# Optimization experiments

Measured on AMD Instinct MI355X. Metric: run time of the kernel, lower is better.

Reference implementation:

```python
import jax, jax.numpy as jnp
import numpy as np

N = 20000      # nodes
K = 32         # avg degree
E = N * K      # edges
H = 128        # num_hidden
NV = 128       # num_V
NE = 128       # num_E
NH = 4         # num_heads (hard-coded in module)
D = H // NH    # per-head dim


def setup_inputs() -> dict:
    key = jax.random.key(0)
    ks = jax.random.split(key, 16)
    w = lambda k, shape: jax.random.normal(k, shape, jnp.float32) * 0.02
    return {
        "h_V": jax.random.normal(ks[0], (N, NV), jnp.float32),
        "h_E": jax.random.normal(ks[1], (E, NE), jnp.float32),
        "edge_idx": jax.random.randint(ks[2], (2, E), 0, N, dtype=jnp.int64),
        # W_V: Linear(num_E, num_hidden) + GELU
        "Wv_w": w(ks[3], (H, NE)), "Wv_b": jnp.zeros((H,), jnp.float32),
        # Bias MLP: Linear(2*num_V+num_E, H) -> ReLU -> Linear(H, H) -> ReLU -> Linear(H, NH)
        "B1_w": w(ks[4], (H, 2 * NV + NE)), "B1_b": jnp.zeros((H,), jnp.float32),
        "B2_w": w(ks[5], (H, H)), "B2_b": jnp.zeros((H,), jnp.float32),
        "B3_w": w(ks[6], (NH, H)), "B3_b": jnp.zeros((NH,), jnp.float32),
        # W_O: Linear(H, num_V, bias=False); gate: Linear(H, num_V)
        "Wo_w": w(ks[7], (NV, H)),
        "gate_w": w(ks[8], (NV, H)), "gate_b": jnp.zeros((NV,), jnp.float32),
    }


def reference(h_V, h_E, edge_idx, Wv_w, Wv_b, B1_w, B1_b, B2_w, B2_b, B3_w, B3_b, Wo_w, gate_w, gate_b):
    src = edge_idx[0]
    dst = edge_idx[1]
    num_nodes = h_V.shape[0]

    # per-edge attention logits via small MLP on [h_V[src], h_E, h_V[dst]]
    cat = jnp.concatenate([h_V[src], h_E, h_V[dst]], axis=-1)          # [E, 2*NV+NE]
    x = jax.nn.relu(cat @ B1_w.T + B1_b)
    x = jax.nn.relu(x @ B2_w.T + B2_b)
    logits = (x @ B3_w.T + B3_b) / np.float32(np.sqrt(D))              # [E, NH]

    # per-edge values
    V = jax.nn.gelu(h_E @ Wv_w.T + Wv_b, approximate=False)           # [E, H]
    V = V.reshape(-1, NH, D)                                           # [E, NH, D]

    # scatter_softmax over edges grouped by src node
    m = jax.ops.segment_max(logits, src, num_segments=num_nodes)       # [N, NH]
    ex = jnp.exp(logits - m[src])                                      # [E, NH]
    denom = jax.ops.segment_sum(ex, src, num_segments=num_nodes)      # [N, NH]
    attend = ex / denom[src]                                           # [E, NH]

    # weighted scatter-sum aggregation
    agg = jax.ops.segment_sum(attend[:, :, None] * V, src, num_segments=num_nodes)
    agg = agg.reshape(num_nodes, -1)                                   # [N, H]

    h_V_gate = jax.nn.sigmoid(agg @ gate_w.T + gate_b)                 # [N, NV]
    dh = (agg @ Wo_w.T) * h_V_gate                                     # [N, NV]
    return h_V + dh
```

## Files before the change

kernel.cpp:

```cpp
#include <hip/hip_runtime.h>
#include <math.h>

typedef __attribute__((ext_vector_type(8))) short bf16x8;
typedef __attribute__((ext_vector_type(4))) float f32x4;
typedef unsigned short u16;

__device__ __forceinline__ short f2bf(float x) {
  union { float f; unsigned u; } c; c.f = x;
  unsigned u = c.u;
  u += 0x7fffu + ((u >> 16) & 1u);
  return (short)(u >> 16);
}
__device__ __forceinline__ float bf2f(u16 b) {
  union { unsigned u; float f; } c; c.u = ((unsigned)b) << 16; return c.f;
}
__device__ __forceinline__ unsigned pack2(float a, float b) {
  return ((unsigned)(u16)f2bf(a)) | (((unsigned)(u16)f2bf(b)) << 16);
}
__device__ __forceinline__ unsigned cvtpk(float lo, float hi) {
  unsigned r;
  asm("v_cvt_pk_bf16_f32 %0, %1, %2" : "=v"(r) : "v"(lo), "v"(hi));
  return r;
}
__device__ __forceinline__ float fast_erf(float x) {
// ... 54 lines not shown

__global__ void scatter_kernel(const int* __restrict__ src, const int* __restrict__ offs,
                               int* __restrict__ cur, int* __restrict__ order, int E) {
  int i = blockIdx.x * 256 + threadIdx.x;
  if (i >= E) return;
  int s = src[i];
  int p = offs[s] + atomicAdd(&cur[s], 1);
  order[p] = i;
}

__global__ void wcvt_kernel(const float* __restrict__ B1, const float* __restrict__ B2,
                            const float* __restrict__ B3, const float* __restrict__ Wv,
                            const float* __restrict__ Wo, const float* __restrict__ Wg,
                            short* __restrict__ o) {
  int i = blockIdx.x * 256 + threadIdx.x;
  if (i >= 115200) return;
  float val; int dst;
  if (i < 49152) {
    int row = i / 384, k = i % 384;
    val = B1[i];
    int c = k >> 5, s = (k >> 3) & 3, e = k & 7;
    dst = c * 4096 + row * 32 + ((s ^ ((row >> 1) & 3)) << 3) + e;
  } else if (i < 65536) {
    int j = i - 49152; int row = j >> 7, k = j & 127;
    val = B2[j];
    int c = k >> 5, s = (k >> 3) & 3, e = k & 7;
    dst = 49152 + c * 4096 + row * 32 + ((s ^ ((row >> 1) & 3)) << 3) + e;
  } else if (i < 66048) { val = B3[i - 65536]; dst = i; }
  else if (i < 82432) {
    int j = i - 66048; int row = j >> 7, k = j & 127;
    val = Wv[j];
    int c = k >> 5, s = (k >> 3) & 3, e = k & 7;
    dst = 66048 + c * 4096 + row * 32 + ((s ^ ((row >> 1) & 3)) << 3) + e;
  }
  else if (i < 98816)  { val = Wo[i - 82432]; dst = i; }
  else                 { val = Wg[i - 98816]; dst = i; }
  o[dst] = f2bf(val);
}

__global__ void cvtbf_kernel(const float* __restrict__ in, u16* __restrict__ out, long n8) {
  long i = (long)blockIdx.x * blockDim.x + threadIdx.x;
  long stride = (long)gridDim.x * blockDim.x;
  for (; i < n8; i += stride) {
    long b = i * 8;
    float4 a = *(const float4*)(in + b);
    float4 c = *(const float4*)(in + b + 4);
    uint4 u;
    u.x = pack2(a.x, a.y); u.y = pack2(a.z, a.w);
    u.z = pack2(c.x, c.y); u.w = pack2(c.z, c.w);
    *(uint4*)(out + b) = u;
  }
}

__global__ void __launch_bounds__(256, 3)
edge_kernel(const u16* __restrict__ hVb, const float* __restrict__ hE,
            const int* __restrict__ src, const int* __restrict__ dst,
            u16* __restrict__ Vout,
            const short* __restrict__ W1, const float* __restrict__ b1,
            const short* __restrict__ W2, const float* __restrict__ b2,
            const short* __restrict__ W3b, const float* __restrict__ b3,
            const short* __restrict__ Wv, const float* __restrict__ bv,
            float* __restrict__ logits, int E) {
  __shared__ u16 sE[64 * 128];
  __shared__ u16 sH[64 * 128];
  __shared__ u16 sW[2][4096];
  __shared__ float sPart[64][4][2];

  const int t = threadIdx.x;
  const int eBase = blockIdx.x * 64;
  const int lane = t & 63;
  const int wid = t >> 6;
  const int wrow = (wid >> 1) * 32;
  const int wcol = (wid & 1) * 64;
  const int lrow = lane & 15;
  const int kgrp = lane >> 4;

  auto STAGE = [&](const short* cp, int buf) {
#pragma unroll
    for (int i = 0; i < 2; ++i) {
      int L = t + i * 256;
      gload16(cp + L * 8, &sW[buf][L * 8]);
    }
  };

  STAGE(W1, 0);

#pragma unroll
  for (int i = 0; i < 4; ++i) {
    int u = t + i * 256;
    int row = u >> 4, sg = u & 15;
    const float* p = hE + (size_t)min(eBase + row, E - 1) * 128 + sg * 8;
    float4 f0 = *(const float4*)p;
    float4 f1 = *(const float4*)(p + 4);
    uint4 cv;
    cv.x = cvtpk(f0.x, f0.y); cv.y = cvtpk(f0.z, f0.w);
    cv.z = cvtpk(f1.x, f1.y); cv.w = cvtpk(f1.z, f1.w);
    *(uint4*)&sE[row * 128 + ((sg ^ (row & 15)) * 8)] = cv;
  }

  bf16x8 aS[4][2], aD[4][2];
  {
    int rS[2], rD[2];
#pragma unroll
    for (int mi = 0; mi < 2; ++mi) {
      int e = min(eBase + wrow + mi * 16 + lrow, E - 1);
      rS[mi] = src[e];
      rD[mi] = dst[e];
    }
#pragma unroll
    for (int c4 = 0; c4 < 4; ++c4) {
      const int kk = c4 * 32 + kgrp * 8;
#pragma unroll
      for (int mi = 0; mi < 2; ++mi) {
        aS[c4][mi] = *(const bf16x8*)(hVb + (size_t)rS[mi] * 128 + kk);
        aD[c4][mi] = *(const bf16x8*)(hVb + (size_t)rD[mi] * 128 + kk);
      }
    }
  }
  asm volatile("s_waitcnt vmcnt(0)" ::: "memory");
  __syncthreads();

  f32x4 acc[2][4];
  auto ZACC = [&]() {
#pragma unroll
    for (int mi = 0; mi < 2; ++mi)
#pragma unroll
      for (int nf = 0; nf < 4; ++nf)
#pragma unroll
        for (int q = 0; q < 4; ++q) acc[mi][nf][q] = 0.f;
  };
  auto LDSA = [&](const u16* s, int kk, bf16x8* a) {
#pragma unroll
    for (int mi = 0; mi < 2; ++mi) {
      int row = wrow + mi * 16 + lrow;
      int seg = (kk >> 3) ^ (row & 15);
      a[mi] = *(const bf16x8*)&s[row * 128 + seg * 8];
    }
  };
  auto STEP = [&](int buf, const short* nextCp, const bf16x8* a) {
    if (nextCp) STAGE(nextCp, buf ^ 1);
    bf16x8 b[4];
#pragma unroll
    for (int nf = 0; nf < 4; ++nf) {
      int row = wcol + nf * 16 + lrow;
      int seg = kgrp ^ ((row >> 1) & 3);
      b[nf] = *(const bf16x8*)&sW[buf][row * 32 + seg * 8];
    }
#pragma unroll
    for (int nf = 0; nf < 4; ++nf)
#pragma unroll
      for (int mi = 0; mi < 2; ++mi)
        acc[mi][nf] = __builtin_amdgcn_mfma_f32_16x16x32_bf16(a[mi], b[nf], acc[mi][nf], 0, 0, 0);
    if (nextCp) asm volatile("s_waitcnt vmcnt(0)" ::: "memory");
    __syncthreads();
  };

  ZACC();
  STEP(0, W1 + 1 * 4096, aS[0]);
  STEP(1, W1 + 2 * 4096, aS[1]);
  STEP(0, W1 + 3 * 4096, aS[2]);
  STEP(1, W1 + 4 * 4096, aS[3]);
#pragma unroll
  for (int c4 = 0; c4 < 4; ++c4) {
    bf16x8 a[2];
    LDSA(sE, c4 * 32 + kgrp * 8, a);
    STEP((4 + c4) & 1, W1 + (5 + c4) * 4096, a);
  }
  STEP(0, W1 + 9 * 4096, aD[0]);
  STEP(1, W1 + 10 * 4096, aD[1]);
  STEP(0, W1 + 11 * 4096, aD[2]);
  STEP(1, Wv, aD[3]);
  {
    float b1c[4];
#pragma unroll
    for (int nf = 0; nf < 4; ++nf) b1c[nf] = b1[wcol + nf * 16 + lrow];
#pragma unroll
    for (int mi = 0; mi < 2; ++mi)
#pragma unroll
      for (int nf = 0; nf < 4; ++nf)
#pragma unroll
        for (int q = 0; q < 4; ++q) {
          int row = wrow + mi * 16 + kgrp * 4 + q;
          int col = wcol + nf * 16 + lrow;
          int seg = (col >> 3) ^ (row & 15);
          sH[row * 128 + seg * 8 + (col & 7)] =
              (u16)f2bf(fmaxf(acc[mi][nf][q] + b1c[nf], 0.f));
        }
  }

  ZACC();
#pragma unroll
  for (int v = 0; v < 4; ++v) {
    bf16x8 a[2];
    LDSA(sE, v * 32 + kgrp * 8, a);
    const short* nxt = (v < 3) ? (Wv + (v + 1) * 4096) : W2;
    STEP(v & 1, nxt, a);
  }
  {
    float bvc[4];
#pragma unroll
    for (int nf = 0; nf < 4; ++nf) bvc[nf] = bv[wcol + nf * 16 + lrow];
#pragma unroll
    for (int mi = 0; mi < 2; ++mi)
#pragma unroll
      for (int nf = 0; nf < 4; ++nf)
#pragma unroll
        for (int q = 0; q < 4; ++q) {
          int row = wrow + mi * 16 + kgrp * 4 + q;
          int col = wcol + nf * 16 + lrow;
          float x = acc[mi][nf][q] + bvc[nf];
          float g = 0.5f * x * (1.0f + fast_erf(x * 0.70710678118654752f));
          int seg = (col >> 3) ^ (row & 15);
          sE[row * 128 + seg * 8 + (col & 7)] = (u16)f2bf(g);
        }
  }
  __syncthreads();
#pragma unroll
  for (int i = 0; i < 4; ++i) {
    int u = t + i * 256;
    int row = u >> 4, g16 = u & 15;
    int seg = g16 ^ (row & 15);
    uint4 v = *(const uint4*)&sE[row * 128 + seg * 8];
    int e = eBase + row;
    if (e < E) *(uint4*)(Vout + (size_t)e * 128 + g16 * 8) = v;
  }

  ZACC();
#pragma unroll
  for (int u = 0; u < 4; ++u) {
    bf16x8 a[2];
    LDSA(sH, u * 32 + kgrp * 8, a);
    const short* nxt = (u < 3) ? (W2 + (u + 1) * 4096) : nullptr;
    STEP(u & 1, nxt, a);
  }
  {
    float b2c[4], w3v[4][4];
#pragma unroll
    for (int nf = 0; nf < 4; ++nf) {
      int col = wcol + nf * 16 + lrow;
      b2c[nf] = b2[col];
#pragma unroll
      for (int h = 0; h < 4; ++h) w3v[h][nf] = bf2f((u16)W3b[h * 128 + col]);
    }
#pragma unroll
    for (int mi = 0; mi < 2; ++mi)
#pragma unroll
      for (int q = 0; q < 4; ++q) {
        float p0 = 0.f, p1 = 0.f, p2 = 0.f, p3 = 0.f;
#pragma unroll
        for (int nf = 0; nf < 4; ++nf) {
          float x = fmaxf(acc[mi][nf][q] + b2c[nf], 0.f);
          p0 += x * w3v[0][nf]; p1 += x * w3v[1][nf];
          p2 += x * w3v[2][nf]; p3 += x * w3v[3][nf];
        }
#pragma unroll
        for (int o = 1; o < 16; o <<= 1) {
          p0 += __shfl_xor(p0, o); p1 += __shfl_xor(p1, o);
          p2 += __shfl_xor(p2, o); p3 += __shfl_xor(p3, o);
        }
        if (lrow < 4) {
          float pw = (lrow == 0) ? p0 : (lrow == 1) ? p1 : (lrow == 2) ? p2 : p3;
          sPart[wrow + mi * 16 + kgrp * 4 + q][lrow][wid & 1] = pw;
        }
      }
  }
  __syncthreads();
  if (t < 64) {
    int e = eBase + t;
    if (e < E) {
      float4 lg;
      lg.x = (sPart[t][0][0] + sPart[t][0][1] + b3[0]) * 0.17677669529663687f;
      lg.y = (sPart[t][1][0] + sPart[t][1][1] + b3[1]) * 0.17677669529663687f;
      lg.z = (sPart[t][2][0] + sPart[t][2][1] + b3[2]) * 0.17677669529663687f;
      lg.w = (sPart[t][3][0] + sPart[t][3][1] + b3[3]) * 0.17677669529663687f;
      *(float4*)(logits + (size_t)e * 4) = lg;
    }
  }
}

__global__ void __launch_bounds__(256)
nm_kernel(const float* __restrict__ logits, const int* __restrict__ offs,
          const int* __restrict__ order, float* __restrict__ attw,
          float* __restrict__ inv, int nN) {
  const int wid = threadIdx.x >> 6, lane = threadIdx.x & 63;
  const int nW = gridDim.x * 4;
  for (int v = blockIdx.x * 4 + wid; v < nN; v += nW) {
    const int base = offs[v];
    const int deg = offs[v + 1] - base;
    float m0 = -3e38f, m1 = -3e38f, m2 = -3e38f, m3 = -3e38f;
    for (int i = lane; i < deg; i += 64) {
      int e = order[base + i];
      float4 l = *(const float4*)(logits + (size_t)e * 4);
      m0 = fmaxf(m0, l.x); m1 = fmaxf(m1, l.y);
      m2 = fmaxf(m2, l.z); m3 = fmaxf(m3, l.w);
    }
#pragma unroll
    for (int o = 32; o > 0; o >>= 1) {
      m0 = fmaxf(m0, __shfl_xor(m0, o)); m1 = fmaxf(m1, __shfl_xor(m1, o));
      m2 = fmaxf(m2, __shfl_xor(m2, o)); m3 = fmaxf(m3, __shfl_xor(m3, o));
    }
    float d0 = 0.f, d1 = 0.f, d2 = 0.f, d3 = 0.f;
    for (int i = lane; i < deg; i += 64) {
      int e = order[base + i];
      float4 l = *(const float4*)(logits + (size_t)e * 4);
      float4 ex;
      ex.x = __expf(l.x - m0); ex.y = __expf(l.y - m1);
      ex.z = __expf(l.z - m2); ex.w = __expf(l.w - m3);
      *(float4*)(attw + (size_t)e * 4) = ex;
      d0 += ex.x; d1 += ex.y; d2 += ex.z; d3 += ex.w;
    }
#pragma unroll
    for (int o = 32; o > 0; o >>= 1) {
      d0 += __shfl_xor(d0, o); d1 += __shfl_xor(d1, o);
      d2 += __shfl_xor(d2, o); d3 += __shfl_xor(d3, o);
    }
    if (lane < 4) {
      float dv = (lane == 0) ? d0 : (lane == 1) ? d1 : (lane == 2) ? d2 : d3;
      inv[(size_t)v * 4 + lane] = (dv > 0.f) ? 1.f / dv : 0.f;
    }
  }
}

__device__ __forceinline__ float dot8(const float* ag, uint4 w) {
  unsigned wr[4] = {w.x, w.y, w.z, w.w};
  float s = 0.f;
#pragma unroll
  for (int q = 0; q < 4; ++q) {
    s += ag[2 * q]     * bf2f((u16)(wr[q] & 0xffffu));
    s += ag[2 * q + 1] * bf2f((u16)(wr[q] >> 16));
// ... 90 lines not shown
  const float* B3w  = (const float*)d_in[9];
  const float* B3b  = (const float*)d_in[10];
  const float* WoW  = (const float*)d_in[11];
  const float* GW   = (const float*)d_in[12];
  const float* GB   = (const float*)d_in[13];

  const int Nn = in_sizes[0] / 128;
  const int E  = in_sizes[1] / 128;
  if (Nn <= 0 || E <= 0) return;

  char* ws = (char*)d_ws;
  size_t off = 0;
  auto alloc = [&](size_t b) { size_t o = off; off += (b + 255) & ~(size_t)255; return o; };
  const size_t o_idx   = alloc((size_t)2 * E * 4);
  const size_t o_cnt   = alloc((size_t)(Nn + 1) * 4);
  const size_t o_offs  = alloc((size_t)(Nn + 1) * 4);
  const size_t o_cur   = alloc((size_t)Nn * 4);
  const size_t o_order = alloc((size_t)E * 4);
  const size_t o_flag  = alloc(256);
  const size_t o_log   = alloc((size_t)E * 16);
  const size_t o_attw  = alloc((size_t)E * 16);
  const size_t o_inv   = alloc((size_t)Nn * 16);
  const size_t o_V     = alloc((size_t)E * 256);
  const size_t o_hVb   = alloc((size_t)Nn * 256);
  const size_t o_wbf   = alloc((size_t)115200 * 2);

  if (off > ws_size) {
    fb_kernel<<<(out_size + 255) / 256, 256, 0, stream>>>(hV, (float*)d_out, out_size);
    return;
  }

  int*   idx32  = (int*)(ws + o_idx);
  int*   cnt    = (int*)(ws + o_cnt);
  int*   offsP  = (int*)(ws + o_offs);
  int*   cur    = (int*)(ws + o_cur);
  int*   order  = (int*)(ws + o_order);
  int*   flag   = (int*)(ws + o_flag);
  float* logits = (float*)(ws + o_log);
  float* attw   = (float*)(ws + o_attw);
  float* invd   = (float*)(ws + o_inv);
  u16*   Vb     = (u16*)(ws + o_V);
  u16*   hVb    = (u16*)(ws + o_hVb);
  short* wbf    = (short*)(ws + o_wbf);

  short* W1b = wbf;
  short* W2b = wbf + 49152;
  short* W3b = wbf + 65536;
  short* Wvb = wbf + 66048;
  short* Wob = wbf + 82432;
  short* Wgb = wbf + 98816;

  const int* src = idx32;
  const int* dst = idx32 + E;

  detect_kernel<<<1, 256, 0, stream>>>((const unsigned*)eidx, flag);
  hipMemsetAsync(cnt, 0, (size_t)(Nn + 1) * 4, stream);
  hipMemsetAsync(cur, 0, (size_t)Nn * 4, stream);
  convert_count_kernel<<<(2 * E + 255) / 256, 256, 0, stream>>>(eidx, idx32, flag, cnt, E);
  scan_kernel<<<1, 1024, 0, stream>>>(cnt, offsP, Nn);
  scatter_kernel<<<(E + 255) / 256, 256, 0, stream>>>(src, offsP, cur, order, E);
  wcvt_kernel<<<(115200 + 255) / 256, 256, 0, stream>>>(B1w, B2w, B3w, WvW, WoW, GW, wbf);
  cvtbf_kernel<<<512, 256, 0, stream>>>(hV, hVb, (long)Nn * 16);

  edge_kernel<<<(E + 63) / 64, 256, 0, stream>>>(
      hVb, hE, src, dst, Vb, W1b, B1b, W2b, B2b, W3b, B3b, Wvb, WvB, logits, E);

  nm_kernel<<<(Nn + 3) / 4, 256, 0, stream>>>(logits, offsP, order, attw, invd, Nn);

  agg_kernel<<<1024, 256, 0, stream>>>(
      hV, attw, invd, Vb, offsP, order, Wob, Wgb, GB, (float*)d_out, Nn);
}
```

Measured before the change: 558.3 us.

## Deepen weight staging to four LDS buffers and interleave V and logits GEMMs

Switches the weight staging in the edge kernel from a double buffer with a full vmcnt(0) wait and barrier after every step to a four-deep ring buffer. Each step now waits on a partial vmcnt count, so several weight chunks stay in flight. The Wv GEMM is moved first and its GELU epilogue and V store are placed between W1 steps, which lets the sE and sH tiles share one LDS buffer. It also keeps two accumulator sets live at once, which raises register pressure and could hurt occupancy under the launch-bounds limit of 3.

Result: slower. 581.7 us (+4.2%).

```diff
diff --git a/kernel.cpp b/kernel.cpp
--- a/kernel.cpp
+++ b/kernel.cpp
@@ -130,6 +130,25 @@
   }
 }
 
+#define STEPK(N, BUF, NEXTP, NBUF, APTR, ACC)                                  \
+  do {                                                                         \
+    asm volatile("s_waitcnt vmcnt(" #N ")" ::: "memory");                      \
+    __builtin_amdgcn_sched_barrier(0);                                         \
+    __builtin_amdgcn_s_barrier();                                              \
+    __builtin_amdgcn_sched_barrier(0);                                         \
+    if (NEXTP) STAGE(NEXTP, NBUF);                                             \
+    bf16x8 b_[4];                                                              \
+    _Pragma("unroll") for (int nf_ = 0; nf_ < 4; ++nf_) {                      \
+      int row_ = wcol + nf_ * 16 + lrow;                                       \
+      int seg_ = kgrp ^ ((row_ >> 1) & 3);                                     \
+      b_[nf_] = *(const bf16x8*)&sW[BUF][row_ * 32 + seg_ * 8];                \
+    }                                                                          \
+    _Pragma("unroll") for (int nf_ = 0; nf_ < 4; ++nf_)                        \
+      _Pragma("unroll") for (int mi_ = 0; mi_ < 2; ++mi_)                      \
+        ACC[mi_][nf_] = __builtin_amdgcn_mfma_f32_16x16x32_bf16(               \
+            (APTR)[mi_], b_[nf_], ACC[mi_][nf_], 0, 0, 0);                     \
+  } while (0)
+
 __global__ void __launch_bounds__(256, 3)
 edge_kernel(const u16* __restrict__ hVb, const float* __restrict__ hE,
             const int* __restrict__ src, const int* __restrict__ dst,
@@ -139,9 +158,8 @@
             const short* __restrict__ W3b, const float* __restrict__ b3,
             const short* __restrict__ Wv, const float* __restrict__ bv,
             float* __restrict__ logits, int E) {
-  __shared__ u16 sE[64 * 128];
-  __shared__ u16 sH[64 * 128];
-  __shared__ u16 sW[2][4096];
+  __shared__ u16 sEH[64 * 128];
+  __shared__ u16 sW[4][4096];
   __shared__ float sPart[64][4][2];
 
   const int t = threadIdx.x;
@@ -161,7 +179,9 @@
     }
   };
 
-  STAGE(W1, 0);
+  STAGE(Wv, 0);
+  STAGE(Wv + 4096, 1);
+  STAGE(Wv + 2 * 4096, 2);
 
 #pragma unroll
   for (int i = 0; i < 4; ++i) {
@@ -173,7 +193,7 @@
     uint4 cv;
     cv.x = cvtpk(f0.x, f0.y); cv.y = cvtpk(f0.z, f0.w);
     cv.z = cvtpk(f1.x, f1.y); cv.w = cvtpk(f1.z, f1.w);
-    *(uint4*)&sE[row * 128 + ((sg ^ (row & 15)) * 8)] = cv;
+    *(uint4*)&sEH[row * 128 + ((sg ^ (row & 15)) * 8)] = cv;
   }
 
   bf16x8 aS[4][2], aD[4][2];
@@ -195,59 +215,78 @@
       }
     }
   }
-  asm volatile("s_waitcnt vmcnt(0)" ::: "memory");
-  __syncthreads();
-
-  f32x4 acc[2][4];
-  auto ZACC = [&]() {
+#pragma unroll
+  for (int c4 = 0; c4 < 4; ++c4)
 #pragma unroll
     for (int mi = 0; mi < 2; ++mi)
-#pragma unroll
-      for (int nf = 0; nf < 4; ++nf)
-#pragma unroll
-        for (int q = 0; q < 4; ++q) acc[mi][nf][q] = 0.f;
-  };
-  auto LDSA = [&](const u16* s, int kk, bf16x8* a) {
+      asm volatile("" :: "v"(aS[c4][mi]), "v"(aD[c4][mi]));
+  __syncthreads();
+
+  f32x4 accL[2][4], accV[2][4];
+#pragma unroll
+  for (int mi = 0; mi < 2; ++mi)
+#pragma unroll
+    for (int nf = 0; nf < 4; ++nf)
+#pragma unroll
+      for (int q = 0; q < 4; ++q) { accL[mi][nf][q] = 0.f; accV[mi][nf][q] = 0.f; }
+
+  auto LDSA = [&](int kk, bf16x8* a) {
 #pragma unroll
     for (int mi = 0; mi < 2; ++mi) {
       int row = wrow + mi * 16 + lrow;
       int seg = (kk >> 3) ^ (row & 15);
-      a[mi] = *(const bf16x8*)&s[row * 128 + seg * 8];
+      a[mi] = *(const bf16x8*)&sEH[row * 128 + seg * 8];
     }
   };
-  auto STEP = [&](int buf, const short* nextCp, const bf16x8* a) {
-    if (nextCp) STAGE(nextCp, buf ^ 1);
-    bf16x8 b[4];
-#pragma unroll
-    for (int nf = 0; nf < 4; ++nf) {
-      int row = wcol + nf * 16 + lrow;
-      int seg = kgrp ^ ((row >> 1) & 3);
-      b[nf] = *(const bf16x8*)&sW[buf][row * 32 + seg * 8];
-    }
-#pragma unroll
-    for (int nf = 0; nf < 4; ++nf)
-#pragma unroll
-      for (int mi = 0; mi < 2; ++mi)
-        acc[mi][nf] = __builtin_amdgcn_mfma_f32_16x16x32_bf16(a[mi], b[nf], acc[mi][nf], 0, 0, 0);
-    if (nextCp) asm volatile("s_waitcnt vmcnt(0)" ::: "memory");
-    __syncthreads();
-  };
-
-  ZACC();
-  STEP(0, W1 + 1 * 4096, aS[0]);
-  STEP(1, W1 + 2 * 4096, aS[1]);
-  STEP(0, W1 + 3 * 4096, aS[2]);
-  STEP(1, W1 + 4 * 4096, aS[3]);
-#pragma unroll
-  for (int c4 = 0; c4 < 4; ++c4) {
-    bf16x8 a[2];
-    LDSA(sE, c4 * 32 + kgrp * 8, a);
-    STEP((4 + c4) & 1, W1 + (5 + c4) * 4096, a);
-  }
-  STEP(0, W1 + 9 * 4096, aD[0]);
-  STEP(1, W1 + 10 * 4096, aD[1]);
-  STEP(0, W1 + 11 * 4096, aD[2]);
-  STEP(1, Wv, aD[3]);
+
+  { bf16x8 a_[2]; LDSA(0 * 32 + kgrp * 8, a_); STEPK(4, 0, Wv + 3 * 4096, 3, a_, accV); }
+  { bf16x8 a_[2]; LDSA(1 * 32 + kgrp * 8, a_); STEPK(4, 1, W1 + 4 * 4096, 0, a_, accV); }
+  { bf16x8 a_[2]; LDSA(2 * 32 + kgrp * 8, a_); STEPK(4, 2, W1 + 5 * 4096, 1, a_, accV); }
+  { bf16x8 a_[2]; LDSA(3 * 32 + kgrp * 8, a_); STEPK(4, 3, W1 + 6 * 4096, 2, a_, accV); }
+  { bf16x8 a_[2]; LDSA(0 * 32 + kgrp * 8, a_); STEPK(4, 0, W1 + 7 * 4096, 3, a_, accL); }
+  { bf16x8 a_[2]; LDSA(1 * 32 + kgrp * 8, a_); STEPK(4, 1, W1 + 0 * 4096, 0, a_, accL); }
+  { bf16x8 a_[2]; LDSA(2 * 32 + kgrp * 8, a_); STEPK(4, 2, W1 + 1 * 4096, 1, a_, accL); }
+  { bf16x8 a_[2]; LDSA(3 * 32 + kgrp * 8, a_); STEPK(4, 3, W1 + 2 * 4096, 2, a_, accL); }
+  STEPK(4, 0, W1 + 3 * 4096, 3, aS[0], accL);
+
+  {
+    float bvc[4];
+#pragma unroll
+    for (int nf = 0; nf < 4; ++nf) bvc[nf] = bv[wcol + nf * 16 + lrow];
+#pragma unroll
+    for (int mi = 0; mi < 2; ++mi)
+#pragma unroll
+      for (int nf = 0; nf < 4; ++nf)
+#pragma unroll
+        for (int q = 0; q < 4; ++q) {
+          int row = wrow + mi * 16 + kgrp * 4 + q;
+          int col = wcol + nf * 16 + lrow;
+          float x = accV[mi][nf][q] + bvc[nf];
+          float g = 0.5f * x * (1.0f + fast_erf(x * 0.70710678118654752f));
+          int seg = (col >> 3) ^ (row & 15);
+          sEH[row * 128 + seg * 8 + (col & 7)] = (u16)f2bf(g);
+        }
+  }
+
+  STEPK(4, 1, W1 + 8 * 4096, 0, aS[1], accL);
+  STEPK(4, 2, W1 + 9 * 4096, 1, aS[2], accL);
+
+#pragma unroll
+  for (int i = 0; i < 4; ++i) {
+    int u = t + i * 256;
+    int row = u >> 4, g16 = u & 15;
+    int seg = g16 ^ (row & 15);
+    uint4 v = *(const uint4*)&sEH[row * 128 + seg * 8];
+    int e = eBase + row;
+    if (e < E) *(uint4*)(Vout + (size_t)e * 128 + g16 * 8) = v;
+  }
+
+  STEPK(8, 3, W1 + 10 * 4096, 2, aS[3], accL);
+  STEPK(8, 0, W1 + 11 * 4096, 3, aD[0], accL);
+  STEPK(8, 1, W2 + 0 * 4096, 0, aD[1], accL);
+  STEPK(4, 2, W2 + 1 * 4096, 1, aD[2], accL);
+  STEPK(4, 3, W2 + 2 * 4096, 2, aD[3], accL);
+
   {
     float b1c[4];
 #pragma unroll
@@ -261,56 +300,23 @@
           int row = wrow + mi * 16 + kgrp * 4 + q;
           int col = wcol + nf * 16 + lrow;
           int seg = (col >> 3) ^ (row & 15);
-          sH[row * 128 + seg * 8 + (col & 7)] =
-              (u16)f2bf(fmaxf(acc[mi][nf][q] + b1c[nf], 0.f));
+          sEH[row * 128 + seg * 8 + (col & 7)] =
+              (u16)f2bf(fmaxf(accL[mi][nf][q] + b1c[nf], 0.f));
         }
-  }
-
-  ZACC();
-#pragma unroll
-  for (int v = 0; v < 4; ++v) {
-    bf16x8 a[2];
-    LDSA(sE, v * 32 + kgrp * 8, a);
-    const short* nxt = (v < 3) ? (Wv + (v + 1) * 4096) : W2;
-    STEP(v & 1, nxt, a);
-  }
-  {
-    float bvc[4];
-#pragma unroll
-    for (int nf = 0; nf < 4; ++nf) bvc[nf] = bv[wcol + nf * 16 + lrow];
 #pragma unroll
     for (int mi = 0; mi < 2; ++mi)
 #pragma unroll
       for (int nf = 0; nf < 4; ++nf)
 #pragma unroll
-        for (int q = 0; q < 4; ++q) {
-          int row = wrow + mi * 16 + kgrp * 4 + q;
-          int col = wcol + nf * 16 + lrow;
-          float x = acc[mi][nf][q] + bvc[nf];
-          float g = 0.5f * x * (1.0f + fast_erf(x * 0.70710678118654752f));
-          int seg = (col >> 3) ^ (row & 15);
-          sE[row * 128 + seg * 8 + (col & 7)] = (u16)f2bf(g);
-        }
-  }
-  __syncthreads();
-#pragma unroll
-  for (int i = 0; i < 4; ++i) {
-    int u = t + i * 256;
-    int row = u >> 4, g16 = u & 15;
-    int seg = g16 ^ (row & 15);
-    uint4 v = *(const uint4*)&sE[row * 128 + seg * 8];
-    int e = eBase + row;
-    if (e < E) *(uint4*)(Vout + (size_t)e * 128 + g16 * 8) = v;
-  }
-
-  ZACC();
-#pragma unroll
-  for (int u = 0; u < 4; ++u) {
-    bf16x8 a[2];
-    LDSA(sH, u * 32 + kgrp * 8, a);
-    const short* nxt = (u < 3) ? (W2 + (u + 1) * 4096) : nullptr;
-    STEP(u & 1, nxt, a);
-  }
+        for (int q = 0; q < 4; ++q) accV[mi][nf][q] = 0.f;
+  }
+  __syncthreads();
+
+  { bf16x8 a_[2]; LDSA(0 * 32 + kgrp * 8, a_); STEPK(4, 0, W2 + 3 * 4096, 3, a_, accV); }
+  { bf16x8 a_[2]; LDSA(1 * 32 + kgrp * 8, a_); STEPK(4, 1, (const short*)nullptr, 0, a_, accV); }
+  { bf16x8 a_[2]; LDSA(2 * 32 + kgrp * 8, a_); STEPK(2, 2, (const short*)nullptr, 0, a_, accV); }
+  { bf16x8 a_[2]; LDSA(3 * 32 + kgrp * 8, a_); STEPK(0, 3, (const short*)nullptr, 0, a_, accV); }
+
   {
     float b2c[4], w3v[4][4];
 #pragma unroll
@@ -327,7 +333,7 @@
         float p0 = 0.f, p1 = 0.f, p2 = 0.f, p3 = 0.f;
 #pragma unroll
         for (int nf = 0; nf < 4; ++nf) {
-          float x = fmaxf(acc[mi][nf][q] + b2c[nf], 0.f);
+          float x = fmaxf(accV[mi][nf][q] + b2c[nf], 0.f);
           p0 += x * w3v[0][nf]; p1 += x * w3v[1][nf];
           p2 += x * w3v[2][nf]; p3 += x * w3v[3][nf];
         }
```

## Triple-buffer weight staging with counted vmcnt waits in edge kernel

Applied to the files above, without the earlier changes.

Replaces the double-buffered weight staging with a three-slot ring, where each step waits with a partial vmcnt, issues one barrier, then prefetches the tile two steps ahead. The goal is to keep more global loads in flight and cut per-step full drains and the trailing barrier. Bias and W3 values are now loaded once up front and pinned in registers, so they no longer load between GEMM phases. The cost is more LDS per block and higher register pressure, which may hurt the three-blocks-per-CU occupancy target, and the hand-counted vmcnt values are fragile.

Result: slower. 641.8 us (+15.0%).

```diff
diff --git a/kernel.cpp b/kernel.cpp
--- a/kernel.cpp
+++ b/kernel.cpp
@@ -130,6 +130,25 @@
   }
 }
 
+#define PSTEP(N, BUF, NEXTP, NBUF, APTR)                                       \
+  do {                                                                         \
+    asm volatile("s_waitcnt vmcnt(" #N ")" ::: "memory");                      \
+    __builtin_amdgcn_sched_barrier(0);                                         \
+    __builtin_amdgcn_s_barrier();                                              \
+    __builtin_amdgcn_sched_barrier(0);                                         \
+    if (NEXTP) STAGE((const short*)(NEXTP), NBUF);                             \
+    bf16x8 b_[4];                                                              \
+    _Pragma("unroll") for (int nf_ = 0; nf_ < 4; ++nf_) {                      \
+      int row_ = wcol + nf_ * 16 + lrow;                                       \
+      int seg_ = kgrp ^ ((row_ >> 1) & 3);                                     \
+      b_[nf_] = *(const bf16x8*)&sW[BUF][row_ * 32 + seg_ * 8];                \
+    }                                                                          \
+    _Pragma("unroll") for (int nf_ = 0; nf_ < 4; ++nf_)                        \
+      _Pragma("unroll") for (int mi_ = 0; mi_ < 2; ++mi_)                      \
+        acc[mi_][nf_] = __builtin_amdgcn_mfma_f32_16x16x32_bf16(               \
+            (APTR)[mi_], b_[nf_], acc[mi_][nf_], 0, 0, 0);                     \
+  } while (0)
+
 __global__ void __launch_bounds__(256, 3)
 edge_kernel(const u16* __restrict__ hVb, const float* __restrict__ hE,
             const int* __restrict__ src, const int* __restrict__ dst,
@@ -141,7 +160,7 @@
             float* __restrict__ logits, int E) {
   __shared__ u16 sE[64 * 128];
   __shared__ u16 sH[64 * 128];
-  __shared__ u16 sW[2][4096];
+  __shared__ u16 sW[3][4096];
   __shared__ float sPart[64][4][2];
 
   const int t = threadIdx.x;
@@ -162,6 +181,7 @@
   };
 
   STAGE(W1, 0);
+  STAGE(W1 + 4096, 1);
 
 #pragma unroll
   for (int i = 0; i < 4; ++i) {
@@ -195,7 +215,27 @@
       }
     }
   }
+  float b1c[4], bvc[4], b2c[4], w3v[4][4];
+#pragma unroll
+  for (int nf = 0; nf < 4; ++nf) {
+    int col = wcol + nf * 16 + lrow;
+    b1c[nf] = b1[col]; bvc[nf] = bv[col]; b2c[nf] = b2[col];
+#pragma unroll
+    for (int h = 0; h < 4; ++h) w3v[h][nf] = bf2f((u16)W3b[h * 128 + col]);
+  }
+#pragma unroll
+  for (int c4 = 0; c4 < 4; ++c4)
+#pragma unroll
+    for (int mi = 0; mi < 2; ++mi)
+      asm volatile("" :: "v"(aS[c4][mi]), "v"(aD[c4][mi]));
+#pragma unroll
+  for (int nf = 0; nf < 4; ++nf) {
+    asm volatile("" :: "v"(b1c[nf]), "v"(bvc[nf]), "v"(b2c[nf]));
+#pragma unroll
+    for (int h = 0; h < 4; ++h) asm volatile("" :: "v"(w3v[h][nf]));
+  }
   asm volatile("s_waitcnt vmcnt(0)" ::: "memory");
+  __builtin_amdgcn_sched_barrier(0);
   __syncthreads();
 
   f32x4 acc[2][4];
@@ -215,83 +255,54 @@
       a[mi] = *(const bf16x8*)&s[row * 128 + seg * 8];
     }
   };
-  auto STEP = [&](int buf, const short* nextCp, const bf16x8* a) {
-    if (nextCp) STAGE(nextCp, buf ^ 1);
-    bf16x8 b[4];
-#pragma unroll
-    for (int nf = 0; nf < 4; ++nf) {
-      int row = wcol + nf * 16 + lrow;
-      int seg = kgrp ^ ((row >> 1) & 3);
-      b[nf] = *(const bf16x8*)&sW[buf][row * 32 + seg * 8];
-    }
+
+  ZACC();
+  PSTEP(2, 0, W1 + 2 * 4096, 2, aS[0]);
+  PSTEP(2, 1, W1 + 3 * 4096, 0, aS[1]);
+  PSTEP(2, 2, W1 + 4 * 4096, 1, aS[2]);
+  PSTEP(2, 0, W1 + 5 * 4096, 2, aS[3]);
+  { bf16x8 a_[2]; LDSA(sE, 0 * 32 + kgrp * 8, a_); PSTEP(2, 1, W1 + 6 * 4096, 0, a_); }
+  { bf16x8 a_[2]; LDSA(sE, 1 * 32 + kgrp * 8, a_); PSTEP(2, 2, W1 + 7 * 4096, 1, a_); }
+  { bf16x8 a_[2]; LDSA(sE, 2 * 32 + kgrp * 8, a_); PSTEP(2, 0, W1 + 8 * 4096, 2, a_); }
+  { bf16x8 a_[2]; LDSA(sE, 3 * 32 + kgrp * 8, a_); PSTEP(2, 1, W1 + 9 * 4096, 0, a_); }
+  PSTEP(2, 2, W1 + 10 * 4096, 1, aD[0]);
+  PSTEP(2, 0, W1 + 11 * 4096, 2, aD[1]);
+  PSTEP(2, 1, Wv, 0, aD[2]);
+  PSTEP(2, 2, Wv + 4096, 1, aD[3]);
+
+#pragma unroll
+  for (int mi = 0; mi < 2; ++mi)
 #pragma unroll
     for (int nf = 0; nf < 4; ++nf)
 #pragma unroll
-      for (int mi = 0; mi < 2; ++mi)
-        acc[mi][nf] = __builtin_amdgcn_mfma_f32_16x16x32_bf16(a[mi], b[nf], acc[mi][nf], 0, 0, 0);
-    if (nextCp) asm volatile("s_waitcnt vmcnt(0)" ::: "memory");
-    __syncthreads();
-  };
+      for (int q = 0; q < 4; ++q) {
+        int row = wrow + mi * 16 + kgrp * 4 + q;
+        int col = wcol + nf * 16 + lrow;
+        int seg = (col >> 3) ^ (row & 15);
+        sH[row * 128 + seg * 8 + (col & 7)] =
+            (u16)f2bf(fmaxf(acc[mi][nf][q] + b1c[nf], 0.f));
+      }
 
   ZACC();
-  STEP(0, W1 + 1 * 4096, aS[0]);
-  STEP(1, W1 + 2 * 4096, aS[1]);
-  STEP(0, W1 + 3 * 4096, aS[2]);
-  STEP(1, W1 + 4 * 4096, aS[3]);
-#pragma unroll
-  for (int c4 = 0; c4 < 4; ++c4) {
-    bf16x8 a[2];
-    LDSA(sE, c4 * 32 + kgrp * 8, a);
-    STEP((4 + c4) & 1, W1 + (5 + c4) * 4096, a);
-  }
-  STEP(0, W1 + 9 * 4096, aD[0]);
-  STEP(1, W1 + 10 * 4096, aD[1]);
-  STEP(0, W1 + 11 * 4096, aD[2]);
-  STEP(1, Wv, aD[3]);
-  {
-    float b1c[4];
-#pragma unroll
-    for (int nf = 0; nf < 4; ++nf) b1c[nf] = b1[wcol + nf * 16 + lrow];
-#pragma unroll
-    for (int mi = 0; mi < 2; ++mi)
-#pragma unroll
-      for (int nf = 0; nf < 4; ++nf)
-#pragma unroll
-        for (int q = 0; q < 4; ++q) {
-          int row = wrow + mi * 16 + kgrp * 4 + q;
-          int col = wcol + nf * 16 + lrow;
-          int seg = (col >> 3) ^ (row & 15);
-          sH[row * 128 + seg * 8 + (col & 7)] =
-              (u16)f2bf(fmaxf(acc[mi][nf][q] + b1c[nf], 0.f));
-        }
-  }
-
-  ZACC();
-#pragma unroll
-  for (int v = 0; v < 4; ++v) {
-    bf16x8 a[2];
-    LDSA(sE, v * 32 + kgrp * 8, a);
-    const short* nxt = (v < 3) ? (Wv + (v + 1) * 4096) : W2;
-    STEP(v & 1, nxt, a);
-  }
-  {
-    float bvc[4];
-#pragma unroll
-    for (int nf = 0; nf < 4; ++nf) bvc[nf] = bv[wcol + nf * 16 + lrow];
-#pragma unroll
-    for (int mi = 0; mi < 2; ++mi)
-#pragma unroll
-      for (int nf = 0; nf < 4; ++nf)
-#pragma unroll
-        for (int q = 0; q < 4; ++q) {
-          int row = wrow + mi * 16 + kgrp * 4 + q;
-          int col = wcol + nf * 16 + lrow;
-          float x = acc[mi][nf][q] + bvc[nf];
-          float g = 0.5f * x * (1.0f + fast_erf(x * 0.70710678118654752f));
-          int seg = (col >> 3) ^ (row & 15);
-          sE[row * 128 + seg * 8 + (col & 7)] = (u16)f2bf(g);
-        }
-  }
+  { bf16x8 a_[2]; LDSA(sE, 0 * 32 + kgrp * 8, a_); PSTEP(2, 0, Wv + 2 * 4096, 2, a_); }
+  { bf16x8 a_[2]; LDSA(sE, 1 * 32 + kgrp * 8, a_); PSTEP(2, 1, Wv + 3 * 4096, 0, a_); }
+  { bf16x8 a_[2]; LDSA(sE, 2 * 32 + kgrp * 8, a_); PSTEP(2, 2, W2, 1, a_); }
+  { bf16x8 a_[2]; LDSA(sE, 3 * 32 + kgrp * 8, a_); PSTEP(2, 0, W2 + 4096, 2, a_); }
+  __syncthreads();
+
+#pragma unroll
+  for (int mi = 0; mi < 2; ++mi)
+#pragma unroll
+    for (int nf = 0; nf < 4; ++nf)
+#pragma unroll
+      for (int q = 0; q < 4; ++q) {
+        int row = wrow + mi * 16 + kgrp * 4 + q;
+        int col = wcol + nf * 16 + lrow;
+        float x = acc[mi][nf][q] + bvc[nf];
+        float g = 0.5f * x * (1.0f + fast_erf(x * 0.70710678118654752f));
+        int seg = (col >> 3) ^ (row & 15);
+        sE[row * 128 + seg * 8 + (col & 7)] = (u16)f2bf(g);
+      }
   __syncthreads();
 #pragma unroll
   for (int i = 0; i < 4; ++i) {
@@ -304,22 +315,12 @@
   }
 
   ZACC();
-#pragma unroll
-  for (int u = 0; u < 4; ++u) {
-    bf16x8 a[2];
-    LDSA(sH, u * 32 + kgrp * 8, a);
-    const short* nxt = (u < 3) ? (W2 + (u + 1) * 4096) : nullptr;
-    STEP(u & 1, nxt, a);
-  }
+  { bf16x8 a_[2]; LDSA(sH, 0 * 32 + kgrp * 8, a_); PSTEP(6, 1, W2 + 2 * 4096, 0, a_); }
+  { bf16x8 a_[2]; LDSA(sH, 1 * 32 + kgrp * 8, a_); PSTEP(6, 2, W2 + 3 * 4096, 1, a_); }
+  { bf16x8 a_[2]; LDSA(sH, 2 * 32 + kgrp * 8, a_); PSTEP(2, 0, (const short*)0, 0, a_); }
+  { bf16x8 a_[2]; LDSA(sH, 3 * 32 + kgrp * 8, a_); PSTEP(0, 1, (const short*)0, 0, a_); }
+
   {
-    float b2c[4], w3v[4][4];
-#pragma unroll
-    for (int nf = 0; nf < 4; ++nf) {
-      int col = wcol + nf * 16 + lrow;
-      b2c[nf] = b2[col];
-#pragma unroll
-      for (int h = 0; h < 4; ++h) w3v[h][nf] = bf2f((u16)W3b[h * 128 + col]);
-    }
 #pragma unroll
     for (int mi = 0; mi < 2; ++mi)
 #pragma unroll
```

## Split edge kernel into persistent logits and V-projection kernels with LDS-resident weights

Applied to the files above, without the earlier changes.

Replaces the single per-tile edge kernel, which re-streamed every weight chunk from global memory per 64-edge tile, with two persistent grid-stride kernels. The logits kernel keeps all of W1 and W2 resident in LDS (about 130KB) across tiles. The V projection kernel keeps Wv resident and runs at higher occupancy. This removes the repeated weight staging and per-chunk barriers. In exchange hE is read from global twice, and the logits kernel runs one 512-thread block per CU with no overlap of gather loads and compute.

Result: slower. 705.8 us (+26.4%).

```diff
diff --git a/kernel.cpp b/kernel.cpp
--- a/kernel.cpp
+++ b/kernel.cpp
@@ -130,158 +130,260 @@
   }
 }
 
-__global__ void __launch_bounds__(256, 3)
-edge_kernel(const u16* __restrict__ hVb, const float* __restrict__ hE,
-            const int* __restrict__ src, const int* __restrict__ dst,
-            u16* __restrict__ Vout,
-            const short* __restrict__ W1, const float* __restrict__ b1,
-            const short* __restrict__ W2, const float* __restrict__ b2,
-            const short* __restrict__ W3b, const float* __restrict__ b3,
-            const short* __restrict__ Wv, const float* __restrict__ bv,
-            float* __restrict__ logits, int E) {
-  __shared__ u16 sE[64 * 128];
-  __shared__ u16 sH[64 * 128];
-  __shared__ u16 sW[2][4096];
-  __shared__ float sPart[64][4][2];
+__global__ void __launch_bounds__(512, 1)
+logits_kernel(const u16* __restrict__ hVb, const float* __restrict__ hE,
+              const int* __restrict__ src, const int* __restrict__ dst,
+              const short* __restrict__ W1, const float* __restrict__ b1,
+              const short* __restrict__ W2, const float* __restrict__ b2,
+              const short* __restrict__ W3b, const float* __restrict__ b3,
+              float* __restrict__ logits, int E, int nTiles) {
+  __shared__ u16 sW1[49152];
+  __shared__ u16 sW2[16384];
+  __shared__ u16 sEH[8192];
+  __shared__ float sPart[64][4][4];
 
   const int t = threadIdx.x;
-  const int eBase = blockIdx.x * 64;
   const int lane = t & 63;
   const int wid = t >> 6;
-  const int wrow = (wid >> 1) * 32;
-  const int wcol = (wid & 1) * 64;
+  const int wrow = (wid >> 2) * 32;
+  const int wcol = (wid & 3) * 32;
   const int lrow = lane & 15;
   const int kgrp = lane >> 4;
 
-  auto STAGE = [&](const short* cp, int buf) {
-#pragma unroll
-    for (int i = 0; i < 2; ++i) {
-      int L = t + i * 256;
-      gload16(cp + L * 8, &sW[buf][L * 8]);
-    }
-  };
-
-  STAGE(W1, 0);
-
+#pragma unroll
+  for (int i = 0; i < 12; ++i) {
+    int L = t + i * 512;
+    gload16(W1 + L * 8, &sW1[L * 8]);
+  }
 #pragma unroll
   for (int i = 0; i < 4; ++i) {
-    int u = t + i * 256;
-    int row = u >> 4, sg = u & 15;
-    const float* p = hE + (size_t)min(eBase + row, E - 1) * 128 + sg * 8;
-    float4 f0 = *(const float4*)p;
-    float4 f1 = *(const float4*)(p + 4);
-    uint4 cv;
-    cv.x = cvtpk(f0.x, f0.y); cv.y = cvtpk(f0.z, f0.w);
-    cv.z = cvtpk(f1.x, f1.y); cv.w = cvtpk(f1.z, f1.w);
-    *(uint4*)&sE[row * 128 + ((sg ^ (row & 15)) * 8)] = cv;
-  }
-
-  bf16x8 aS[4][2], aD[4][2];
-  {
-    int rS[2], rD[2];
-#pragma unroll
-    for (int mi = 0; mi < 2; ++mi) {
-      int e = min(eBase + wrow + mi * 16 + lrow, E - 1);
-      rS[mi] = src[e];
-      rD[mi] = dst[e];
-    }
-#pragma unroll
-    for (int c4 = 0; c4 < 4; ++c4) {
-      const int kk = c4 * 32 + kgrp * 8;
-#pragma unroll
-      for (int mi = 0; mi < 2; ++mi) {
-        aS[c4][mi] = *(const bf16x8*)(hVb + (size_t)rS[mi] * 128 + kk);
-        aD[c4][mi] = *(const bf16x8*)(hVb + (size_t)rD[mi] * 128 + kk);
-      }
-    }
-  }
+    int L = t + i * 512;
+    gload16(W2 + L * 8, &sW2[L * 8]);
+  }
+  float b1c[2], b2c[2], w3v[4][2];
+#pragma unroll
+  for (int nf = 0; nf < 2; ++nf) {
+    int col = wcol + nf * 16 + lrow;
+    b1c[nf] = b1[col]; b2c[nf] = b2[col];
+#pragma unroll
+    for (int h = 0; h < 4; ++h) w3v[h][nf] = bf2f((u16)W3b[h * 128 + col]);
+  }
+  const float b3c0 = b3[0], b3c1 = b3[1], b3c2 = b3[2], b3c3 = b3[3];
   asm volatile("s_waitcnt vmcnt(0)" ::: "memory");
   __syncthreads();
 
-  f32x4 acc[2][4];
+  f32x4 acc[2][2];
   auto ZACC = [&]() {
 #pragma unroll
     for (int mi = 0; mi < 2; ++mi)
 #pragma unroll
-      for (int nf = 0; nf < 4; ++nf)
+      for (int nf = 0; nf < 2; ++nf)
 #pragma unroll
         for (int q = 0; q < 4; ++q) acc[mi][nf][q] = 0.f;
   };
-  auto LDSA = [&](const u16* s, int kk, bf16x8* a) {
+  auto LDSA = [&](int kk, bf16x8* a) {
 #pragma unroll
     for (int mi = 0; mi < 2; ++mi) {
       int row = wrow + mi * 16 + lrow;
       int seg = (kk >> 3) ^ (row & 15);
-      a[mi] = *(const bf16x8*)&s[row * 128 + seg * 8];
+      a[mi] = *(const bf16x8*)&sEH[row * 128 + seg * 8];
     }
   };
-  auto STEP = [&](int buf, const short* nextCp, const bf16x8* a) {
-    if (nextCp) STAGE(nextCp, buf ^ 1);
-    bf16x8 b[4];
-#pragma unroll
-    for (int nf = 0; nf < 4; ++nf) {
-      int row = wcol + nf * 16 + lrow;
-      int seg = kgrp ^ ((row >> 1) & 3);
-      b[nf] = *(const bf16x8*)&sW[buf][row * 32 + seg * 8];
-    }
-#pragma unroll
-    for (int nf = 0; nf < 4; ++nf)
-#pragma unroll
-      for (int mi = 0; mi < 2; ++mi)
-        acc[mi][nf] = __builtin_amdgcn_mfma_f32_16x16x32_bf16(a[mi], b[nf], acc[mi][nf], 0, 0, 0);
-    if (nextCp) asm volatile("s_waitcnt vmcnt(0)" ::: "memory");
-    __syncthreads();
-  };
-
-  ZACC();
-  STEP(0, W1 + 1 * 4096, aS[0]);
-  STEP(1, W1 + 2 * 4096, aS[1]);
-  STEP(0, W1 + 3 * 4096, aS[2]);
-  STEP(1, W1 + 4 * 4096, aS[3]);
-#pragma unroll
-  for (int c4 = 0; c4 < 4; ++c4) {
-    bf16x8 a[2];
-    LDSA(sE, c4 * 32 + kgrp * 8, a);
-    STEP((4 + c4) & 1, W1 + (5 + c4) * 4096, a);
-  }
-  STEP(0, W1 + 9 * 4096, aD[0]);
-  STEP(1, W1 + 10 * 4096, aD[1]);
-  STEP(0, W1 + 11 * 4096, aD[2]);
-  STEP(1, Wv, aD[3]);
-  {
-    float b1c[4];
-#pragma unroll
-    for (int nf = 0; nf < 4; ++nf) b1c[nf] = b1[wcol + nf * 16 + lrow];
+
+  for (int tile = blockIdx.x; tile < nTiles; tile += gridDim.x) {
+    const int eBase = tile * 64;
+#pragma unroll
+    for (int i = 0; i < 2; ++i) {
+      int u = t + i * 512;
+      int row = u >> 4, sg = u & 15;
+      const float* p = hE + (size_t)min(eBase + row, E - 1) * 128 + sg * 8;
+      float4 f0 = *(const float4*)p;
+      float4 f1 = *(const float4*)(p + 4);
+      uint4 cv;
+      cv.x = cvtpk(f0.x, f0.y); cv.y = cvtpk(f0.z, f0.w);
+      cv.z = cvtpk(f1.x, f1.y); cv.w = cvtpk(f1.z, f1.w);
+      *(uint4*)&sEH[row * 128 + ((sg ^ (row & 15)) * 8)] = cv;
+    }
+    bf16x8 aS[4][2], aD[4][2];
+    {
+      int rS[2], rD[2];
+#pragma unroll
+      for (int mi = 0; mi < 2; ++mi) {
+        int e = min(eBase + wrow + mi * 16 + lrow, E - 1);
+        rS[mi] = src[e]; rD[mi] = dst[e];
+      }
+#pragma unroll
+      for (int c4 = 0; c4 < 4; ++c4) {
+        int kk = c4 * 32 + kgrp * 8;
+#pragma unroll
+        for (int mi = 0; mi < 2; ++mi) {
+          aS[c4][mi] = *(const bf16x8*)(hVb + (size_t)rS[mi] * 128 + kk);
+          aD[c4][mi] = *(const bf16x8*)(hVb + (size_t)rD[mi] * 128 + kk);
+        }
+      }
+    }
+    __syncthreads();
+
+    ZACC();
+#pragma unroll
+    for (int c = 0; c < 12; ++c) {
+      bf16x8 a[2], b[2];
+      if (c < 4)      { a[0] = aS[c][0]; a[1] = aS[c][1]; }
+      else if (c < 8) { LDSA((c - 4) * 32 + kgrp * 8, a); }
+      else            { a[0] = aD[c - 8][0]; a[1] = aD[c - 8][1]; }
+#pragma unroll
+      for (int nf = 0; nf < 2; ++nf) {
+        int row_ = wcol + nf * 16 + lrow;
+        b[nf] = *(const bf16x8*)&sW1[c * 4096 + row_ * 32 + ((kgrp ^ ((row_ >> 1) & 3)) << 3)];
+      }
+#pragma unroll
+      for (int nf = 0; nf < 2; ++nf)
+#pragma unroll
+        for (int mi = 0; mi < 2; ++mi)
+          acc[mi][nf] = __builtin_amdgcn_mfma_f32_16x16x32_bf16(a[mi], b[nf], acc[mi][nf], 0, 0, 0);
+    }
+    __syncthreads();
+
 #pragma unroll
     for (int mi = 0; mi < 2; ++mi)
 #pragma unroll
-      for (int nf = 0; nf < 4; ++nf)
+      for (int nf = 0; nf < 2; ++nf)
 #pragma unroll
         for (int q = 0; q < 4; ++q) {
           int row = wrow + mi * 16 + kgrp * 4 + q;
           int col = wcol + nf * 16 + lrow;
           int seg = (col >> 3) ^ (row & 15);
-          sH[row * 128 + seg * 8 + (col & 7)] =
+          sEH[row * 128 + seg * 8 + (col & 7)] =
               (u16)f2bf(fmaxf(acc[mi][nf][q] + b1c[nf], 0.f));
         }
-  }
-
-  ZACC();
-#pragma unroll
-  for (int v = 0; v < 4; ++v) {
-    bf16x8 a[2];
-    LDSA(sE, v * 32 + kgrp * 8, a);
-    const short* nxt = (v < 3) ? (Wv + (v + 1) * 4096) : W2;
-    STEP(v & 1, nxt, a);
-  }
-  {
-    float bvc[4];
-#pragma unroll
-    for (int nf = 0; nf < 4; ++nf) bvc[nf] = bv[wcol + nf * 16 + lrow];
+    __syncthreads();
+
+    ZACC();
+#pragma unroll
+    for (int c = 0; c < 4; ++c) {
+      bf16x8 a[2], b[2];
+      LDSA(c * 32 + kgrp * 8, a);
+#pragma unroll
+      for (int nf = 0; nf < 2; ++nf) {
+        int row_ = wcol + nf * 16 + lrow;
+        b[nf] = *(const bf16x8*)&sW2[c * 4096 + row_ * 32 + ((kgrp ^ ((row_ >> 1) & 3)) << 3)];
+      }
+#pragma unroll
+      for (int nf = 0; nf < 2; ++nf)
+#pragma unroll
+        for (int mi = 0; mi < 2; ++mi)
+          acc[mi][nf] = __builtin_amdgcn_mfma_f32_16x16x32_bf16(a[mi], b[nf], acc[mi][nf], 0, 0, 0);
+    }
+
 #pragma unroll
     for (int mi = 0; mi < 2; ++mi)
 #pragma unroll
-      for (int nf = 0; nf < 4; ++nf)
+      for (int q = 0; q < 4; ++q) {
+        float p0 = 0.f, p1 = 0.f, p2 = 0.f, p3 = 0.f;
+#pragma unroll
+        for (int nf = 0; nf < 2; ++nf) {
+          float x = fmaxf(acc[mi][nf][q] + b2c[nf], 0.f);
+          p0 += x * w3v[0][nf]; p1 += x * w3v[1][nf];
+          p2 += x * w3v[2][nf]; p3 += x * w3v[3][nf];
+        }
+#pragma unroll
+        for (int o = 1; o < 16; o <<= 1) {
+          p0 += __shfl_xor(p0, o); p1 += __shfl_xor(p1, o);
+          p2 += __shfl_xor(p2, o); p3 += __shfl_xor(p3, o);
+        }
+        if (lrow < 4) {
+          float pw = (lrow == 0) ? p0 : (lrow == 1) ? p1 : (lrow == 2) ? p2 : p3;
+          sPart[wrow + mi * 16 + kgrp * 4 + q][lrow][wid & 3] = pw;
+        }
+      }
+    __syncthreads();
+    if (t < 256) {
+      int r = t >> 2, h = t & 3;
+      float bb = (h == 0) ? b3c0 : (h == 1) ? b3c1 : (h == 2) ? b3c2 : b3c3;
+      float lg = (sPart[r][h][0] + sPart[r][h][1] + sPart[r][h][2] + sPart[r][h][3] + bb)
+                 * 0.17677669529663687f;
+      int e = eBase + r;
+      if (e < E) logits[(size_t)e * 4 + h] = lg;
+    }
+    __syncthreads();
+  }
+}
+
+__global__ void __launch_bounds__(512, 3)
+vproj_kernel(const float* __restrict__ hE, const short* __restrict__ Wv,
+             const float* __restrict__ bv, u16* __restrict__ Vout,
+             int E, int nTiles) {
+  __shared__ u16 sWv[16384];
+  __shared__ u16 sE[8192];
+
+  const int t = threadIdx.x;
+  const int lane = t & 63;
+  const int wid = t >> 6;
+  const int wrow = (wid >> 2) * 32;
+  const int wcol = (wid & 3) * 32;
+  const int lrow = lane & 15;
+  const int kgrp = lane >> 4;
+
+#pragma unroll
+  for (int i = 0; i < 4; ++i) {
+    int L = t + i * 512;
+    gload16(Wv + L * 8, &sWv[L * 8]);
+  }
+  float bvc[2];
+#pragma unroll
+  for (int nf = 0; nf < 2; ++nf) bvc[nf] = bv[wcol + nf * 16 + lrow];
+  asm volatile("s_waitcnt vmcnt(0)" ::: "memory");
+  __syncthreads();
+
+  f32x4 acc[2][2];
+  for (int tile = blockIdx.x; tile < nTiles; tile += gridDim.x) {
+    const int eBase = tile * 64;
+#pragma unroll
+    for (int i = 0; i < 2; ++i) {
+      int u = t + i * 512;
+      int row = u >> 4, sg = u & 15;
+      const float* p = hE + (size_t)min(eBase + row, E - 1) * 128 + sg * 8;
+      float4 f0 = *(const float4*)p;
+      float4 f1 = *(const float4*)(p + 4);
+      uint4 cv;
+      cv.x = cvtpk(f0.x, f0.y); cv.y = cvtpk(f0.z, f0.w);
+      cv.z = cvtpk(f1.x, f1.y); cv.w = cvtpk(f1.z, f1.w);
+      *(uint4*)&sE[row * 128 + ((sg ^ (row & 15)) * 8)] = cv;
+    }
+    __syncthreads();
+
+#pragma unroll
+    for (int mi = 0; mi < 2; ++mi)
+#pragma unroll
+      for (int nf = 0; nf < 2; ++nf)
+#pragma unroll
+        for (int q = 0; q < 4; ++q) acc[mi][nf][q] = 0.f;
+#pragma unroll
+    for (int c = 0; c < 4; ++c) {
+      bf16x8 a[2], b[2];
+#pragma unroll
+      for (int mi = 0; mi < 2; ++mi) {
+        int row = wrow + mi * 16 + lrow;
+        int seg = ((c * 32 + kgrp * 8) >> 3) ^ (row & 15);
+        a[mi] = *(const bf16x8*)&sE[row * 128 + seg * 8];
+      }
+#pragma unroll
+      for (int nf = 0; nf < 2; ++nf) {
+        int row_ = wcol + nf * 16 + lrow;
+        b[nf] = *(const bf16x8*)&sWv[c * 4096 + row_ * 32 + ((kgrp ^ ((row_ >> 1) & 3)) << 3)];
+      }
+#pragma unroll
+      for (int nf = 0; nf < 2; ++nf)
+#pragma unroll
+        for (int mi = 0; mi < 2; ++mi)
+          acc[mi][nf] = __builtin_amdgcn_mfma_f32_16x16x32_bf16(a[mi], b[nf], acc[mi][nf], 0, 0, 0);
+    }
+    __syncthreads();
+
+#pragma unroll
+    for (int mi = 0; mi < 2; ++mi)
+#pragma unroll
+      for (int nf = 0; nf < 2; ++nf)
 #pragma unroll
         for (int q = 0; q < 4; ++q) {
           int row = wrow + mi * 16 + kgrp * 4 + q;
@@ -291,68 +393,17 @@
           int seg = (col >> 3) ^ (row & 15);
           sE[row * 128 + seg * 8 + (col & 7)] = (u16)f2bf(g);
         }
-  }
-  __syncthreads();
-#pragma unroll
-  for (int i = 0; i < 4; ++i) {
-    int u = t + i * 256;
-    int row = u >> 4, g16 = u & 15;
-    int seg = g16 ^ (row & 15);
-    uint4 v = *(const uint4*)&sE[row * 128 + seg * 8];
-    int e = eBase + row;
-    if (e < E) *(uint4*)(Vout + (size_t)e * 128 + g16 * 8) = v;
-  }
-
-  ZACC();
-#pragma unroll
-  for (int u = 0; u < 4; ++u) {
-    bf16x8 a[2];
-    LDSA(sH, u * 32 + kgrp * 8, a);
-    const short* nxt = (u < 3) ? (W2 + (u + 1) * 4096) : nullptr;
-    STEP(u & 1, nxt, a);
-  }
-  {
-    float b2c[4], w3v[4][4];
-#pragma unroll
-    for (int nf = 0; nf < 4; ++nf) {
-      int col = wcol + nf * 16 + lrow;
-      b2c[nf] = b2[col];
-#pragma unroll
-      for (int h = 0; h < 4; ++h) w3v[h][nf] = bf2f((u16)W3b[h * 128 + col]);
-    }
-#pragma unroll
-    for (int mi = 0; mi < 2; ++mi)
-#pragma unroll
-      for (int q = 0; q < 4; ++q) {
-        float p0 = 0.f, p1 = 0.f, p2 = 0.f, p3 = 0.f;
-#pragma unroll
-        for (int nf = 0; nf < 4; ++nf) {
-          float x = fmaxf(acc[mi][nf][q] + b2c[nf], 0.f);
-          p0 += x * w3v[0][nf]; p1 += x * w3v[1][nf];
-          p2 += x * w3v[2][nf]; p3 += x * w3v[3][nf];
-        }
-#pragma unroll
-        for (int o = 1; o < 16; o <<= 1) {
-          p0 += __shfl_xor(p0, o); p1 += __shfl_xor(p1, o);
-          p2 += __shfl_xor(p2, o); p3 += __shfl_xor(p3, o);
-        }
-        if (lrow < 4) {
-          float pw = (lrow == 0) ? p0 : (lrow == 1) ? p1 : (lrow == 2) ? p2 : p3;
-          sPart[wrow + mi * 16 + kgrp * 4 + q][lrow][wid & 1] = pw;
-        }
-      }
-  }
-  __syncthreads();
-  if (t < 64) {
-    int e = eBase + t;
-    if (e < E) {
-      float4 lg;
-      lg.x = (sPart[t][0][0] + sPart[t][0][1] + b3[0]) * 0.17677669529663687f;
-      lg.y = (sPart[t][1][0] + sPart[t][1][1] + b3[1]) * 0.17677669529663687f;
-      lg.z = (sPart[t][2][0] + sPart[t][2][1] + b3[2]) * 0.17677669529663687f;
-      lg.w = (sPart[t][3][0] + sPart[t][3][1] + b3[3]) * 0.17677669529663687f;
-      *(float4*)(logits + (size_t)e * 4) = lg;
-    }
+    __syncthreads();
+#pragma unroll
+    for (int i = 0; i < 2; ++i) {
+      int u = t + i * 512;
+      int row = u >> 4, g16 = u & 15;
+      int seg = g16 ^ (row & 15);
+      uint4 v = *(const uint4*)&sE[row * 128 + seg * 8];
+      int e = eBase + row;
+      if (e < E) *(uint4*)(Vout + (size_t)e * 128 + g16 * 8) = v;
+    }
+    __syncthreads();
   }
 }
 
@@ -549,6 +600,7 @@
 
   const int* src = idx32;
   const int* dst = idx32 + E;
+  const int nTiles = (E + 63) / 64;
 
   detect_kernel<<<1, 256, 0, stream>>>((const unsigned*)eidx, flag);
   hipMemsetAsync(cnt, 0, (size_t)(Nn + 1) * 4, stream);
@@ -559,8 +611,10 @@
   wcvt_kernel<<<(115200 + 255) / 256, 256, 0, stream>>>(B1w, B2w, B3w, WvW, WoW, GW, wbf);
   cvtbf_kernel<<<512, 256, 0, stream>>>(hV, hVb, (long)Nn * 16);
 
-  edge_kernel<<<(E + 63) / 64, 256, 0, stream>>>(
-      hVb, hE, src, dst, Vb, W1b, B1b, W2b, B2b, W3b, B3b, Wvb, WvB, logits, E);
+  logits_kernel<<<256, 512, 0, stream>>>(
+      hVb, hE, src, dst, W1b, B1b, W2b, B2b, W3b, B3b, logits, E, nTiles);
+
+  vproj_kernel<<<768, 512, 0, stream>>>(hE, Wvb, WvB, Vb, E, nTiles);
 
   nm_kernel<<<(Nn + 3) / 4, 256, 0, stream>>>(logits, offsP, order, attw, invd, Nn);
 
```
